# Kernel tuning notes

Measured on AMD Instinct MI355X. Metric: run time of the kernel, lower is better.

Reference implementation:

```python
import jax, jax.numpy as jnp
import numpy as np

N_NODES = 20000
D_FEAT = 256
N_SUPPORT = 3
N_EDGES = 320000
OUT_DIM = 256


def setup_inputs() -> dict:
    key = jax.random.key(0)
    k1, k2, k3, k4, k5 = jax.random.split(key, 5)
    x = jax.random.normal(k1, (N_NODES, D_FEAT), dtype=jnp.float32)
    edge_src = jax.random.randint(k2, (N_SUPPORT, N_EDGES), 0, N_NODES, dtype=jnp.int64 if jax.config.jax_enable_x64 else jnp.int32).astype(jnp.int32)
    edge_dst = jax.random.randint(k3, (N_SUPPORT, N_EDGES), 0, N_NODES, dtype=jnp.int32)
    edge_w = jax.random.uniform(k4, (N_SUPPORT, N_EDGES), dtype=jnp.float32)
    # dense weight over concatenated supports: (support * input_dim, output_dim)
    W = jax.random.normal(k5, (N_SUPPORT * D_FEAT, OUT_DIM), dtype=jnp.float32) * (1.0 / np.sqrt(N_SUPPORT * D_FEAT))
    return {"x": x, "edge_src": edge_src, "edge_dst": edge_dst, "edge_w": edge_w, "W": W}


def reference(x, edge_src, edge_dst, edge_w, W):
    # supports_i = A_i @ x  (sparse adjacency as weighted edge list, per support)
    n = x.shape[0]
    supports = []
    for s in range(edge_src.shape[0]):  # small fixed number of relations
        msgs = x[edge_src[s]] * edge_w[s][:, None]              # [E, d]
        supports.append(jax.ops.segment_sum(msgs, edge_dst[s], num_segments=n))
    h = jnp.concatenate(supports, axis=1)                        # [N, support*d]
    # activation='linear' -> identity; bias=False
    return h @ W                                                 # [N, output_dim]
```

## Files before the change

kernel.cpp:

```cpp
#include <hip/hip_runtime.h>

#define N_NODES 20000
#define D_FEAT 256
#define N_SUPPORT 3
#define N_EDGES 320000
#define OUT_DIM 256
#define TOTAL_E (N_SUPPORT * N_EDGES)
#define CAP 64
#define CAPX 16
#define NWIN 8
#define KDIM (N_SUPPORT * D_FEAT)
#define NBUCKET (N_SUPPORT * N_NODES)
#define GM_ROWS 128
#define GM_BLOCKS ((N_NODES + GM_ROWS - 1) / GM_ROWS)

typedef __attribute__((ext_vector_type(8))) short short8;
typedef __attribute__((ext_vector_type(8))) unsigned short ushort8;
typedef __attribute__((ext_vector_type(4))) float f32x4;

__device__ inline unsigned short f2bf(float f) {
    unsigned int u = __float_as_uint(f);
    u += 0x7fff + ((u >> 16) & 1);
    return (unsigned short)(u >> 16);
}

#define NB_X (N_NODES / 16)
#define NB_W (N_SUPPORT * D_FEAT)
#define NB_F (TOTAL_E / 256)

__global__ void __launch_bounds__(256) prep1(const float* __restrict__ x, const float* __restrict__ W,
        unsigned int* __restrict__ xq, float* __restrict__ scl, unsigned short* __restrict__ wt) {
    const int bid = blockIdx.x;
    const int tid = threadIdx.x;
    if (bid < NB_X) {
        const int wid = tid >> 6;
        const int lane = tid & 63;
        const int row0 = bid * 16 + wid * 4;
        float4 v[4];
        float m[4];
#pragma unroll
        for (int r = 0; r < 4; ++r) {
            v[r] = ((const float4*)x)[(size_t)(row0 + r) * 64 + lane];
            m[r] = fmaxf(fmaxf(fabsf(v[r].x), fabsf(v[r].y)), fmaxf(fabsf(v[r].z), fabsf(v[r].w)));
        }
#pragma unroll
        for (int d = 1; d < 64; d <<= 1) {
#pragma unroll
            for (int r = 0; r < 4; ++r) m[r] = fmaxf(m[r], __shfl_xor(m[r], d, 64));
        }
#pragma unroll
        for (int r = 0; r < 4; ++r) {
            const float inv = (m[r] > 0.f) ? 127.0f / m[r] : 0.f;
            int q0 = (int)rintf(v[r].x * inv) + 128;
            int q1 = (int)rintf(v[r].y * inv) + 128;
            int q2 = (int)rintf(v[r].z * inv) + 128;
            int q3 = (int)rintf(v[r].w * inv) + 128;
            unsigned int pk = (unsigned int)q0 | ((unsigned int)q1 << 8)
                            | ((unsigned int)q2 << 16) | ((unsigned int)q3 << 24);
            xq[(size_t)(row0 + r) * 64 + lane] = pk;
            if (lane == 0) scl[row0 + r] = m[r] * (1.0f / 127.0f);
        }
    } else {
        const int row = bid - NB_X;
        const int s = row >> 8, k = row & 255;
        wt[((size_t)s * OUT_DIM + tid) * D_FEAT + k] = f2bf(W[(size_t)row * OUT_DIM + tid]);
    }
}

__global__ void __launch_bounds__(256) fill_win(const int* __restrict__ src,
        const int* __restrict__ dst, const float* __restrict__ w, const float* __restrict__ scl,
        int* __restrict__ cur8, unsigned int* __restrict__ ep1) {
    const int i = blockIdx.x * 256 + threadIdx.x;
    if (i >= TOTAL_E) return;
    const int win = blockIdx.x & (NWIN - 1);
    const int s = i / N_EDGES;
    const int sv = src[i];
    const int b = s * N_NODES + dst[i];
    const int pos = atomicAdd(&cur8[win * NBUCKET + b], 1);
    if (pos < CAPX) {
        const float wq = w[i] * scl[sv];
        ep1[((size_t)win * NBUCKET + b) * CAPX + pos] =
            (unsigned int)sv | (((unsigned int)f2bf(wq)) << 16);
    }
}

__global__ void __launch_bounds__(256) compact(const int* __restrict__ cur8,
        const unsigned int* __restrict__ ep1, int* __restrict__ cnt2,
        unsigned int* __restrict__ ep2) {
    const int b = blockIdx.x * 8 + (threadIdx.x >> 5);
    const int l32 = threadIdx.x & 31;

    int myc = 0;
    if (l32 < NWIN) {
        int c = cur8[l32 * NBUCKET + b];
        myc = (c > CAPX) ? CAPX : c;
    }
    int cx[NWIN], off[NWIN];
    int tot = 0;
#pragma unroll
    for (int xw = 0; xw < NWIN; ++xw) {
        cx[xw] = __shfl(myc, xw, 32);
        off[xw] = tot;
        tot += cx[xw];
    }
    if (tot > CAP) tot = CAP;

    for (int i = l32; i < tot; i += 32) {
        int xw = 0, idx = 0;
#pragma unroll
        for (int t = 0; t < NWIN; ++t) {
            if (i >= off[t] && i < off[t] + cx[t]) { xw = t; idx = i - off[t]; }
        }
        ep2[(size_t)b * CAP + i] = ep1[((size_t)xw * NBUCKET + b) * CAPX + idx];
    }
    if (l32 == 0) cnt2[b] = tot;
}

__global__ void __launch_bounds__(256) aggregate(
        const unsigned char* __restrict__ xq, const int* __restrict__ cnt2,
        const unsigned int* __restrict__ epack, unsigned short* __restrict__ hb) {
    const int b = blockIdx.x * 8 + (threadIdx.x >> 5);
    const int l32 = threadIdx.x & 31;
    const int xoff = l32 * 8;
    const int s = b / N_NODES;
    const int node = b - s * N_NODES;

    int c = cnt2[b]; if (c > CAP) c = CAP;
    const unsigned int* ep = epack + (size_t)b * CAP;

    float a[8];
#pragma unroll
    for (int j = 0; j < 8; ++j) a[j] = 0.f;
    float sw = 0.f;

    int it = 0;
    for (; it + 3 < c; it += 4) {
        const uint4 pk = *(const uint4*)(ep + it);
        const uint2 u0 = *(const uint2*)(xq + ((size_t)(pk.x & 0xFFFFu) << 8) + xoff);
        const uint2 u1 = *(const uint2*)(xq + ((size_t)(pk.y & 0xFFFFu) << 8) + xoff);
        const uint2 u2 = *(const uint2*)(xq + ((size_t)(pk.z & 0xFFFFu) << 8) + xoff);
        const uint2 u3 = *(const uint2*)(xq + ((size_t)(pk.w & 0xFFFFu) << 8) + xoff);
        const float w0 = __uint_as_float(pk.x & 0xFFFF0000u);
        const float w1 = __uint_as_float(pk.y & 0xFFFF0000u);
        const float w2 = __uint_as_float(pk.z & 0xFFFF0000u);
        const float w3 = __uint_as_float(pk.w & 0xFFFF0000u);
        sw += w0 + w1 + w2 + w3;
#pragma unroll
        for (int j = 0; j < 4; ++j) {
            const int sh = 8 * j;
            a[j]     += w0 * (float)((u0.x >> sh) & 0xffu) + w1 * (float)((u1.x >> sh) & 0xffu)
                      + w2 * (float)((u2.x >> sh) & 0xffu) + w3 * (float)((u3.x >> sh) & 0xffu);
            a[4 + j] += w0 * (float)((u0.y >> sh) & 0xffu) + w1 * (float)((u1.y >> sh) & 0xffu)
                      + w2 * (float)((u2.y >> sh) & 0xffu) + w3 * (float)((u3.y >> sh) & 0xffu);
        }
    }
    for (; it < c; ++it) {
        const unsigned int pe = ep[it];
        const uint2 u = *(const uint2*)(xq + ((size_t)(pe & 0xFFFFu) << 8) + xoff);
        const float wv = __uint_as_float(pe & 0xFFFF0000u);
        sw += wv;
#pragma unroll
        for (int j = 0; j < 4; ++j) {
            const int sh = 8 * j;
            a[j]     += wv * (float)((u.x >> sh) & 0xffu);
            a[4 + j] += wv * (float)((u.y >> sh) & 0xffu);
        }
    }

    ushort8 o;
    const float bias = 128.f * sw;
#pragma unroll
    for (int j = 0; j < 8; ++j) o[j] = f2bf(a[j] - bias);
    *(ushort8*)(hb + (size_t)node * KDIM + s * D_FEAT + xoff) = o;
}

__global__ void __launch_bounds__(512) gemm_h(
        const unsigned short* __restrict__ hb, const unsigned short* __restrict__ wt,
        float* __restrict__ out) {
    __shared__ unsigned short bs[OUT_DIM][136];
    const int n0 = blockIdx.x * GM_ROWS;
    const int wid = threadIdx.x >> 6;
    const int lane = threadIdx.x & 63;
    const int cit = lane & 15;
    const int kgrp = (lane >> 4) * 8;
    const bool valid = (n0 + wid * 16) < N_NODES;
    const int arow_idx = valid ? (n0 + wid * 16 + cit) : 0;
    const short* arow = (const short*)hb + (size_t)arow_idx * KDIM + kgrp;

    f32x4 acc[16];
#pragma unroll
    for (int j = 0; j < 16; ++j) acc[j] = (f32x4){0.f, 0.f, 0.f, 0.f};

    for (int kc = 0; kc < 6; ++kc) {
        const int s = kc >> 1;
        const int kb = (kc & 1) * 128;
        if (kc) __syncthreads();
        for (int i = threadIdx.x; i < 4096; i += 512) {
            const int n = i >> 4;
            const int k8 = (i & 15) << 3;
            *(ushort8*)&bs[n][k8] =
                *(const ushort8*)(wt + ((size_t)s * OUT_DIM + n) * D_FEAT + kb + k8);
        }
        __syncthreads();

#pragma unroll
        for (int ks = 0; ks < 4; ++ks) {
            short8 av = *(const short8*)(arow + kc * 128 + ks * 32);
#pragma unroll
            for (int nt = 0; nt < 16; ++nt) {
                short8 bv = *(const short8*)&bs[nt * 16 + cit][ks * 32 + kgrp];
                acc[nt] = __builtin_amdgcn_mfma_f32_16x16x32_bf16(av, bv, acc[nt], 0, 0, 0);
            }
        }
    }

    if (valid) {
        const int rbase = (lane >> 4) * 4;
#pragma unroll
        for (int nt = 0; nt < 16; ++nt) {
            const int col = nt * 16 + cit;
#pragma unroll
            for (int r = 0; r < 4; ++r) {
                out[(size_t)(n0 + wid * 16 + rbase + r) * OUT_DIM + col] = acc[nt][r];
            }
        }
    }
}

extern "C" void kernel_launch(void* const* d_in, const int* in_sizes, int n_in,
                              void* d_out, int out_size, void* d_ws, size_t ws_size,
                              hipStream_t stream) {
    const float* x        = (const float*)d_in[0];
    const int*   edge_src = (const int*)d_in[1];
    const int*   edge_dst = (const int*)d_in[2];
    const float* edge_w   = (const float*)d_in[3];
    const float* W        = (const float*)d_in[4];
    float* out = (float*)d_out;

    char* ws = (char*)d_ws;
    unsigned int*   xq    = (unsigned int*)(ws);
    float*          scl   = (float*)(ws + 5120000);
    unsigned short* wt    = (unsigned short*)(ws + 5200000);
    int*            cur8  = (int*)(ws + 5593216);
    int*            cnt2  = (int*)(ws + 7513216);
    unsigned int*   ep2   = (unsigned int*)(ws + 7753216);
    unsigned int*   ep1   = (unsigned int*)(ws + 23113216);
    unsigned short* hb    = (unsigned short*)(ws + 23113216);

    hipMemsetAsync(cur8, 0, 1920000, stream);

    prep1<<<NB_X + NB_W, 256, 0, stream>>>(x, W, xq, scl, wt);
    fill_win<<<NB_F, 256, 0, stream>>>(edge_src, edge_dst, edge_w, scl, cur8, ep1);
    compact<<<NBUCKET / 8, 256, 0, stream>>>(cur8, ep1, cnt2, ep2);

    aggregate<<<NBUCKET / 8, 256, 0, stream>>>((const unsigned char*)xq, cnt2, ep2, hb);

    gemm_h<<<GM_BLOCKS, 512, 0, stream>>>(hb, wt, out);
}
```

Baseline: 129.7 us.

## Fuse compaction into aggregate by reading per-window edge buckets directly

Removes the compact kernel and its intermediate ep2/cnt2 buffers; aggregate now reads the per-window counters and slots directly from ep1. The ep1 and cur8 layouts become bucket-major (window innermost), so each bucket's windows are contiguous and aggregate can prefetch the first four entries of every window with one vector load each. The cost is predicated work for empty slots, since all eight windows are always processed with four entries each. It also drops the total cap of 64 edges per bucket that compact used to enforce.

```diff
diff --git a/kernel.cpp b/kernel.cpp
--- a/kernel.cpp
+++ b/kernel.cpp
@@ -6,7 +6,6 @@
 #define N_EDGES 320000
 #define OUT_DIM 256
 #define TOTAL_E (N_SUPPORT * N_EDGES)
-#define CAP 64
 #define CAPX 16
 #define NWIN 8
 #define KDIM (N_SUPPORT * D_FEAT)
@@ -76,94 +75,69 @@
     const int s = i / N_EDGES;
     const int sv = src[i];
     const int b = s * N_NODES + dst[i];
-    const int pos = atomicAdd(&cur8[win * NBUCKET + b], 1);
+    const int pos = atomicAdd(&cur8[b * NWIN + win], 1);
     if (pos < CAPX) {
         const float wq = w[i] * scl[sv];
-        ep1[((size_t)win * NBUCKET + b) * CAPX + pos] =
+        ep1[(size_t)b * (NWIN * CAPX) + win * CAPX + pos] =
             (unsigned int)sv | (((unsigned int)f2bf(wq)) << 16);
     }
 }
 
-__global__ void __launch_bounds__(256) compact(const int* __restrict__ cur8,
-        const unsigned int* __restrict__ ep1, int* __restrict__ cnt2,
-        unsigned int* __restrict__ ep2) {
-    const int b = blockIdx.x * 8 + (threadIdx.x >> 5);
-    const int l32 = threadIdx.x & 31;
-
-    int myc = 0;
-    if (l32 < NWIN) {
-        int c = cur8[l32 * NBUCKET + b];
-        myc = (c > CAPX) ? CAPX : c;
-    }
-    int cx[NWIN], off[NWIN];
-    int tot = 0;
-#pragma unroll
-    for (int xw = 0; xw < NWIN; ++xw) {
-        cx[xw] = __shfl(myc, xw, 32);
-        off[xw] = tot;
-        tot += cx[xw];
-    }
-    if (tot > CAP) tot = CAP;
-
-    for (int i = l32; i < tot; i += 32) {
-        int xw = 0, idx = 0;
-#pragma unroll
-        for (int t = 0; t < NWIN; ++t) {
-            if (i >= off[t] && i < off[t] + cx[t]) { xw = t; idx = i - off[t]; }
-        }
-        ep2[(size_t)b * CAP + i] = ep1[((size_t)xw * NBUCKET + b) * CAPX + idx];
-    }
-    if (l32 == 0) cnt2[b] = tot;
+#define PROC(p) {                                                              \
+    const unsigned int sv_ = (p) & 0xFFFFu;                                    \
+    const uint2 u_ = *(const uint2*)(xq + ((size_t)sv_ << 8) + xoff);          \
+    const float wv_ = __uint_as_float((p) & 0xFFFF0000u);                      \
+    sw += wv_;                                                                 \
+    _Pragma("unroll")                                                          \
+    for (int j = 0; j < 4; ++j) {                                              \
+        const int sh = 8 * j;                                                  \
+        a[j]     += wv_ * (float)((u_.x >> sh) & 0xffu);                       \
+        a[4 + j] += wv_ * (float)((u_.y >> sh) & 0xffu);                       \
+    }                                                                          \
 }
 
 __global__ void __launch_bounds__(256) aggregate(
-        const unsigned char* __restrict__ xq, const int* __restrict__ cnt2,
-        const unsigned int* __restrict__ epack, unsigned short* __restrict__ hb) {
+        const unsigned char* __restrict__ xq, const int* __restrict__ cur8,
+        const unsigned int* __restrict__ ep1, unsigned short* __restrict__ hb) {
     const int b = blockIdx.x * 8 + (threadIdx.x >> 5);
     const int l32 = threadIdx.x & 31;
     const int xoff = l32 * 8;
     const int s = b / N_NODES;
     const int node = b - s * N_NODES;
 
-    int c = cnt2[b]; if (c > CAP) c = CAP;
-    const unsigned int* ep = epack + (size_t)b * CAP;
+    int myc = 0;
+    if (l32 < NWIN) {
+        int c = cur8[b * NWIN + l32];
+        myc = (c > CAPX) ? CAPX : c;
+    }
+    int c[NWIN];
+#pragma unroll
+    for (int w = 0; w < NWIN; ++w) c[w] = __shfl(myc, w, 32);
+
+    const unsigned int* eb = ep1 + (size_t)b * (NWIN * CAPX);
+
+    uint4 g[NWIN];
+#pragma unroll
+    for (int w = 0; w < NWIN; ++w) g[w] = *(const uint4*)(eb + w * CAPX);
 
     float a[8];
 #pragma unroll
     for (int j = 0; j < 8; ++j) a[j] = 0.f;
     float sw = 0.f;
 
-    int it = 0;
-    for (; it + 3 < c; it += 4) {
-        const uint4 pk = *(const uint4*)(ep + it);
-        const uint2 u0 = *(const uint2*)(xq + ((size_t)(pk.x & 0xFFFFu) << 8) + xoff);
-        const uint2 u1 = *(const uint2*)(xq + ((size_t)(pk.y & 0xFFFFu) << 8) + xoff);
-        const uint2 u2 = *(const uint2*)(xq + ((size_t)(pk.z & 0xFFFFu) << 8) + xoff);
-        const uint2 u3 = *(const uint2*)(xq + ((size_t)(pk.w & 0xFFFFu) << 8) + xoff);
-        const float w0 = __uint_as_float(pk.x & 0xFFFF0000u);
-        const float w1 = __uint_as_float(pk.y & 0xFFFF0000u);
-        const float w2 = __uint_as_float(pk.z & 0xFFFF0000u);
-        const float w3 = __uint_as_float(pk.w & 0xFFFF0000u);
-        sw += w0 + w1 + w2 + w3;
-#pragma unroll
-        for (int j = 0; j < 4; ++j) {
-            const int sh = 8 * j;
-            a[j]     += w0 * (float)((u0.x >> sh) & 0xffu) + w1 * (float)((u1.x >> sh) & 0xffu)
-                      + w2 * (float)((u2.x >> sh) & 0xffu) + w3 * (float)((u3.x >> sh) & 0xffu);
-            a[4 + j] += w0 * (float)((u0.y >> sh) & 0xffu) + w1 * (float)((u1.y >> sh) & 0xffu)
-                      + w2 * (float)((u2.y >> sh) & 0xffu) + w3 * (float)((u3.y >> sh) & 0xffu);
-        }
-    }
-    for (; it < c; ++it) {
-        const unsigned int pe = ep[it];
-        const uint2 u = *(const uint2*)(xq + ((size_t)(pe & 0xFFFFu) << 8) + xoff);
-        const float wv = __uint_as_float(pe & 0xFFFF0000u);
-        sw += wv;
-#pragma unroll
-        for (int j = 0; j < 4; ++j) {
-            const int sh = 8 * j;
-            a[j]     += wv * (float)((u.x >> sh) & 0xffu);
-            a[4 + j] += wv * (float)((u.y >> sh) & 0xffu);
+#pragma unroll
+    for (int w = 0; w < NWIN; ++w) {
+        const int cw = c[w];
+        const unsigned int p0 = (cw > 0) ? g[w].x : 0u;
+        const unsigned int p1 = (cw > 1) ? g[w].y : 0u;
+        const unsigned int p2 = (cw > 2) ? g[w].z : 0u;
+        const unsigned int p3 = (cw > 3) ? g[w].w : 0u;
+        PROC(p0); PROC(p1); PROC(p2); PROC(p3);
+        if (cw > 4) {
+            for (int it = 4; it < cw; ++it) {
+                const unsigned int pe = eb[w * CAPX + it];
+                PROC(pe);
+            }
         }
     }
 
@@ -242,18 +216,15 @@
     float*          scl   = (float*)(ws + 5120000);
     unsigned short* wt    = (unsigned short*)(ws + 5200000);
     int*            cur8  = (int*)(ws + 5593216);
-    int*            cnt2  = (int*)(ws + 7513216);
-    unsigned int*   ep2   = (unsigned int*)(ws + 7753216);
-    unsigned int*   ep1   = (unsigned int*)(ws + 23113216);
-    unsigned short* hb    = (unsigned short*)(ws + 23113216);
+    unsigned int*   ep1   = (unsigned int*)(ws + 7513216);
+    unsigned short* hb    = (unsigned short*)(ws + 38233216);
 
     hipMemsetAsync(cur8, 0, 1920000, stream);
 
     prep1<<<NB_X + NB_W, 256, 0, stream>>>(x, W, xq, scl, wt);
     fill_win<<<NB_F, 256, 0, stream>>>(edge_src, edge_dst, edge_w, scl, cur8, ep1);
-    compact<<<NBUCKET / 8, 256, 0, stream>>>(cur8, ep1, cnt2, ep2);
-
-    aggregate<<<NBUCKET / 8, 256, 0, stream>>>((const unsigned char*)xq, cnt2, ep2, hb);
+
+    aggregate<<<NBUCKET / 8, 256, 0, stream>>>((const unsigned char*)xq, cur8, ep1, hb);
 
     gemm_h<<<GM_BLOCKS, 512, 0, stream>>>(hb, wt, out);
 }
```

Result: slower. 144.6 us (+11.5%).
